# Performance work log

Measured on AMD Instinct MI355X. Metric: run time of the kernel, lower is better.

## Reference

```python
import jax, jax.numpy as jnp
import numpy as np

N = 65536   # batch_size * timeseries
D = 512     # feature dim of h_real
K = 64      # n_clusters


def setup_inputs() -> dict:
    key = jax.random.key(0)
    k1, k2 = jax.random.split(key)
    h_real = jax.random.normal(k1, (N, D), dtype=jnp.float32)
    # F is an (approximately) orthogonal projection parameter [N, K].
    F = jax.random.normal(k2, (N, K), dtype=jnp.float32)
    return {"h_real": h_real, "F": F}


def reference(h_real, F):
    # Original: WTW = h h^T (N x N); loss = trace(WTW) - trace(F^T WTW F).
    # Algebraically identical reduced form, never materializing the N x N Gram:
    #   trace(h h^T) = sum(h * h)
    #   trace(F^T h h^T F) = ||F^T h||_F^2
    tr_wtw = jnp.sum(h_real * h_real)
    G = F.T @ h_real                      # [K, D] skinny GEMM
    tr_proj = jnp.sum(G * G)
    return tr_wtw - tr_proj
```

## Files before the change

### kernel.cpp

```cpp
#include <hip/hip_runtime.h>
#include <hip/hip_fp16.h>

#define N_TOT 65536
#define D_DIM 512
#define K_DIM 64
#define NC    32
#define HT_S  40
#define GSZ   (K_DIM * D_DIM)

typedef __bf16   bf16x8 __attribute__((ext_vector_type(8)));
typedef float    f32x4  __attribute__((ext_vector_type(4)));
typedef _Float16 half8  __attribute__((ext_vector_type(8)));

__device__ __forceinline__ unsigned int pack_bf16(float a, float b) {
    union { float f; unsigned int u; } x, y;
    x.f = a; y.f = b;
    unsigned int lo = (x.u + 0x7fffu + ((x.u >> 16) & 1u)) >> 16;
    unsigned int hi = (y.u + 0x7fffu + ((y.u >> 16) & 1u)) >> 16;
    return lo | (hi << 16);
}

extern "C" __global__ void __launch_bounds__(1024)
k1_partial(const float* __restrict__ h, const float* __restrict__ F,
           float* __restrict__ trw_out, unsigned short* __restrict__ gpart,
           float* __restrict__ out, int rowsPerBlock) {
    __shared__ unsigned short ht[D_DIM * HT_S];
    __shared__ unsigned short Ft[K_DIM * HT_S];
    __shared__ float red[16];

    const int tid = threadIdx.x;
    const int b   = blockIdx.x;
    if (b == 0 && tid == 0) out[0] = 0.0f;

    const int row0    = b * rowsPerBlock;
    const int nChunks = rowsPerBlock / NC;

    const int sd = tid & 511;
    const int sp = tid >> 9;
    const int fk = tid & 63;
    const int fp = tid >> 6;
    const int wave = tid >> 6;
    const int lane = tid & 63;
    const int m    = lane & 15;
    const int q    = lane >> 4;

    f32x4 acc[4][2];
    #pragma unroll
    for (int kt = 0; kt < 4; ++kt)
        #pragma unroll
        for (int dt = 0; dt < 2; ++dt)
            acc[kt][dt] = (f32x4){0.f, 0.f, 0.f, 0.f};

    float trw = 0.f;

    for (int c = 0; c < nChunks; ++c) {
        const int r0 = row0 + c * NC;
        const float* hb = h + (size_t)r0 * D_DIM;
        #pragma unroll
        for (int it = 0; it < 8; ++it) {
            const int r = it * 4 + sp * 2;
            float v0 = hb[(size_t)r       * D_DIM + sd];
            float v1 = hb[(size_t)(r + 1) * D_DIM + sd];
            trw += v0 * v0 + v1 * v1;
            *(unsigned int*)&ht[sd * HT_S + r] = pack_bf16(v0, v1);
        }
        {
            const float* fb = F + (size_t)r0 * K_DIM;
            const int r = fp * 2;
            float v0 = fb[(size_t)r       * K_DIM + fk];
            float v1 = fb[(size_t)(r + 1) * K_DIM + fk];
            *(unsigned int*)&Ft[fk * HT_S + r] = pack_bf16(v0, v1);
        }
        __syncthreads();
        bf16x8 bfrag[2], afrag[4];
        #pragma unroll
        for (int dt = 0; dt < 2; ++dt)
            bfrag[dt] = *(const bf16x8*)&ht[(wave * 32 + dt * 16 + m) * HT_S + q * 8];
        #pragma unroll
        for (int kt = 0; kt < 4; ++kt)
            afrag[kt] = *(const bf16x8*)&Ft[(kt * 16 + m) * HT_S + q * 8];
        #pragma unroll
        for (int kt = 0; kt < 4; ++kt)
            #pragma unroll
            for (int dt = 0; dt < 2; ++dt)
                acc[kt][dt] = __builtin_amdgcn_mfma_f32_16x16x32_bf16(
                    afrag[kt], bfrag[dt], acc[kt][dt], 0, 0, 0);
        __syncthreads();
    }

    unsigned short* gp = gpart + (size_t)b * GSZ;
    #pragma unroll
    for (int kt = 0; kt < 4; ++kt)
        #pragma unroll
        for (int dt = 0; dt < 2; ++dt)
            #pragma unroll
            for (int r = 0; r < 4; ++r) {
                const int k = kt * 16 + q * 4 + r;
                const int d = wave * 32 + dt * 16 + m;
                __half hv = __float2half(acc[kt][dt][r]);
                gp[k * D_DIM + d] = *(unsigned short*)&hv;
            }

    #pragma unroll
    for (int off = 32; off > 0; off >>= 1) trw += __shfl_down(trw, off, 64);
    if (lane == 0) red[wave] = trw;
    __syncthreads();
    if (tid == 0) {
        float s = 0.f;
        #pragma unroll
        for (int w = 0; w < 16; ++w) s += red[w];
        trw_out[b] = s;
    }
}

extern "C" __global__ void __launch_bounds__(1024)
k2_reduce(const float* __restrict__ trw, const unsigned short* __restrict__ gpart,
          float* __restrict__ out, int P) {
    __shared__ float sh[4 * 256 * 8];
    __shared__ float red[4];

    const int sub   = threadIdx.x >> 8;
    const int local = threadIdx.x & 255;
    const int tt    = blockIdx.x * 256 + local;

    float g[8];
    #pragma unroll
    for (int j = 0; j < 8; ++j) g[j] = 0.f;

    const unsigned short* base = gpart + (size_t)tt * 8;
    for (int b = sub; b < P; b += 4) {
        half8 v = *(const half8*)(base + (size_t)b * GSZ);
        #pragma unroll
        for (int j = 0; j < 8; ++j) g[j] += (float)v[j];
    }
    #pragma unroll
    for (int j = 0; j < 8; ++j) sh[(sub * 256 + local) * 8 + j] = g[j];
    __syncthreads();

    float s = 0.f;
    if (threadIdx.x < 256) {
        #pragma unroll
        for (int j = 0; j < 8; ++j) {
            float gg = sh[(0 * 256 + local) * 8 + j] + sh[(1 * 256 + local) * 8 + j]
                     + sh[(2 * 256 + local) * 8 + j] + sh[(3 * 256 + local) * 8 + j];
            s -= gg * gg;
        }
        if (tt < P) s += trw[tt];
        #pragma unroll
        for (int off = 32; off > 0; off >>= 1) s += __shfl_down(s, off, 64);
        if ((threadIdx.x & 63) == 0) red[threadIdx.x >> 6] = s;
    }
    __syncthreads();
    if (threadIdx.x == 0)
        atomicAdd(out, red[0] + red[1] + red[2] + red[3]);
}

extern "C" void kernel_launch(void* const* d_in, const int* in_sizes, int n_in,
                              void* d_out, int out_size, void* d_ws, size_t ws_size,
                              hipStream_t stream) {
    const float* h = (const float*)d_in[0];
    const float* F = (const float*)d_in[1];
    float* out = (float*)d_out;

    int P = 256;
    while (P > 1 && (size_t)4096 + (size_t)P * (GSZ * 2) > ws_size) P >>= 1;
    const int rowsPerBlock = N_TOT / P;

    float* trw = (float*)d_ws;
    unsigned short* gpart = (unsigned short*)((char*)d_ws + 4096);

    hipLaunchKernelGGL(k1_partial, dim3(P), dim3(1024), 0, stream,
                       h, F, trw, gpart, out, rowsPerBlock);
    hipLaunchKernelGGL(k2_reduce, dim3(16), dim3(1024), 0, stream,
                       trw, gpart, out, P);
}
```

Measured before the change: 223.0 us.

## Double-buffer LDS staging and load h as float2 to overlap loads with MFMA

Splits the LDS tiles for h and F into two buffers. The next chunk is staged while MFMAs run on the current one, which removes one of the two barriers per chunk. The h loads are widened to float2, with each thread writing two transposed columns. This doubles LDS use to about 90KB per block, and the staging writes happen in the same instruction stream as the MFMA reads, so any overlap depends on how the compiler schedules them.

```diff
diff --git a/kernel.cpp b/kernel.cpp
--- a/kernel.cpp
+++ b/kernel.cpp
@@ -24,8 +24,8 @@
 k1_partial(const float* __restrict__ h, const float* __restrict__ F,
            float* __restrict__ trw_out, unsigned short* __restrict__ gpart,
            float* __restrict__ out, int rowsPerBlock) {
-    __shared__ unsigned short ht[D_DIM * HT_S];
-    __shared__ unsigned short Ft[K_DIM * HT_S];
+    __shared__ unsigned short ht[2][D_DIM * HT_S];
+    __shared__ unsigned short Ft[2][K_DIM * HT_S];
     __shared__ float red[16];
 
     const int tid = threadIdx.x;
@@ -35,8 +35,8 @@
     const int row0    = b * rowsPerBlock;
     const int nChunks = rowsPerBlock / NC;
 
-    const int sd = tid & 511;
-    const int sp = tid >> 9;
+    const int d2 = tid & 255;
+    const int rp = tid >> 8;
     const int fk = tid & 63;
     const int fp = tid >> 6;
     const int wave = tid >> 6;
@@ -53,39 +53,45 @@
 
     float trw = 0.f;
 
+    auto stage = [&](int c, int p) {
+        const int r0 = row0 + c * NC;
+        const float2* hb = (const float2*)(h + (size_t)r0 * D_DIM);
+        #pragma unroll
+        for (int it = 0; it < 4; ++it) {
+            const int r = it * 8 + rp * 2;
+            float2 v0 = hb[(size_t)r       * 256 + d2];
+            float2 v1 = hb[(size_t)(r + 1) * 256 + d2];
+            trw += v0.x * v0.x + v0.y * v0.y + v1.x * v1.x + v1.y * v1.y;
+            *(unsigned int*)&ht[p][(2 * d2)     * HT_S + r] = pack_bf16(v0.x, v1.x);
+            *(unsigned int*)&ht[p][(2 * d2 + 1) * HT_S + r] = pack_bf16(v0.y, v1.y);
+        }
+        const float* fb = F + (size_t)r0 * K_DIM;
+        const int r = fp * 2;
+        float v0 = fb[(size_t)r       * K_DIM + fk];
+        float v1 = fb[(size_t)(r + 1) * K_DIM + fk];
+        *(unsigned int*)&Ft[p][fk * HT_S + r] = pack_bf16(v0, v1);
+    };
+
+    stage(0, 0);
+
     for (int c = 0; c < nChunks; ++c) {
-        const int r0 = row0 + c * NC;
-        const float* hb = h + (size_t)r0 * D_DIM;
-        #pragma unroll
-        for (int it = 0; it < 8; ++it) {
-            const int r = it * 4 + sp * 2;
-            float v0 = hb[(size_t)r       * D_DIM + sd];
-            float v1 = hb[(size_t)(r + 1) * D_DIM + sd];
-            trw += v0 * v0 + v1 * v1;
-            *(unsigned int*)&ht[sd * HT_S + r] = pack_bf16(v0, v1);
-        }
-        {
-            const float* fb = F + (size_t)r0 * K_DIM;
-            const int r = fp * 2;
-            float v0 = fb[(size_t)r       * K_DIM + fk];
-            float v1 = fb[(size_t)(r + 1) * K_DIM + fk];
-            *(unsigned int*)&Ft[fk * HT_S + r] = pack_bf16(v0, v1);
-        }
         __syncthreads();
+        if (c + 1 < nChunks) stage(c + 1, (c + 1) & 1);
+
+        const int p = c & 1;
         bf16x8 bfrag[2], afrag[4];
         #pragma unroll
         for (int dt = 0; dt < 2; ++dt)
-            bfrag[dt] = *(const bf16x8*)&ht[(wave * 32 + dt * 16 + m) * HT_S + q * 8];
+            bfrag[dt] = *(const bf16x8*)&ht[p][(wave * 32 + dt * 16 + m) * HT_S + q * 8];
         #pragma unroll
         for (int kt = 0; kt < 4; ++kt)
-            afrag[kt] = *(const bf16x8*)&Ft[(kt * 16 + m) * HT_S + q * 8];
+            afrag[kt] = *(const bf16x8*)&Ft[p][(kt * 16 + m) * HT_S + q * 8];
         #pragma unroll
         for (int kt = 0; kt < 4; ++kt)
             #pragma unroll
             for (int dt = 0; dt < 2; ++dt)
                 acc[kt][dt] = __builtin_amdgcn_mfma_f32_16x16x32_bf16(
                     afrag[kt], bfrag[dt], acc[kt][dt], 0, 0, 0);
-        __syncthreads();
     }
 
     unsigned short* gp = gpart + (size_t)b * GSZ;
```

Measured after the change: 226.0 us. Within noise of the previous version (+1.4%).
